# Kernel optimization log

Hardware: AMD Instinct MI355X
Metric: run time of the kernel (lower is better)

The kernel has to match this reference:

```python
import jax, jax.numpy as jnp
import numpy as np

ALPHA = 0.2  # leaky_relu negative slope


def setup_inputs() -> dict:
    key = jax.random.key(0)
    ks = jax.random.split(key, 6)
    N, E, F_IN, F_OUT, E_DIM = 50000, 800000, 256, 256, 64
    h = jax.random.normal(ks[0], (N, F_IN), dtype=jnp.float32)
    e_feat = jax.random.normal(ks[1], (E, E_DIM), dtype=jnp.float32)
    W = jax.random.normal(ks[2], (F_OUT, F_IN), dtype=jnp.float32) * (1.0 / np.sqrt(F_IN))
    A = jax.random.normal(ks[3], (1, 2 * F_OUT + E_DIM), dtype=jnp.float32) * 0.05
    src = jax.random.randint(ks[4], (E,), 0, N, dtype=jnp.int32)
    dst = jax.random.randint(ks[5], (E,), 0, N, dtype=jnp.int32)
    return {"h": h, "e_feat": e_feat, "W": W, "A": A, "src": src, "dst": dst}


def reference(h, e_feat, W, A, src, dst):
    N = h.shape[0]
    F_OUT = W.shape[0]
    # equation (1): node projection
    z = h @ W.T  # [N, F_OUT]
    z_src = z[src]  # [E, F_OUT]
    z_dst = z[dst]  # [E, F_OUT]
    # equation (2): per-edge attention logit = attn_fc([z_src, z_dst, e_feat])
    # split A to avoid materializing the [E, 2F+De] concat
    a_src, a_dst, a_e = A[0, :F_OUT], A[0, F_OUT:2 * F_OUT], A[0, 2 * F_OUT:]
    logits = z_src @ a_src + z_dst @ a_dst + e_feat @ a_e  # [E]
    e = jax.nn.leaky_relu(logits, ALPHA)
    # equations (3)&(4): segment-softmax over incoming edges per destination
    m = jax.ops.segment_max(e, dst, num_segments=N)  # [N]
    ex = jnp.exp(e - m[dst])
    denom = jax.ops.segment_sum(ex, dst, num_segments=N)  # [N]
    alpha = ex / denom[dst]  # [E]
    h_out = jax.ops.segment_sum(alpha[:, None] * z_src, dst, num_segments=N)
    return h_out
```

## Files before the change

kernel.cpp:

```cpp
#include <hip/hip_runtime.h>
#include <hip/hip_bf16.h>

#define FDIM 256
#define EDIM 64
#define LEAKY 0.2f

#define BM 128
#define BN 128
#define BK 32

typedef __attribute__((ext_vector_type(8))) short bfrag;
typedef __attribute__((ext_vector_type(4))) float f4acc;

__device__ __forceinline__ unsigned f2bf(float x){
    unsigned u = __float_as_uint(x);
    return (u + 0x7FFFu + ((u >> 16) & 1u)) >> 16;
}
__device__ __forceinline__ float bf2f(unsigned b){
    return __uint_as_float(b << 16);
}
__device__ __forceinline__ unsigned pack_hi(float x, float y, float& hx, float& hy){
    unsigned bx = f2bf(x), by = f2bf(y);
    hx = bf2f(bx); hy = bf2f(by);
    return bx | (by << 16);
}
__device__ __forceinline__ unsigned pack_lo(float rx, float ry){
    return f2bf(rx) | (f2bf(ry) << 16);
}

__device__ __forceinline__ void atomic_max_float(float* addr, float val){
    if (val >= 0.f) atomicMax((int*)addr, __float_as_int(val));
    else            atomicMin((unsigned int*)addr, (unsigned int)__float_as_int(val));
}

__global__ void k_init(float* __restrict__ m, float* __restrict__ s_src,
                       float* __restrict__ s_dst, int* __restrict__ counts, int N){
    int i = blockIdx.x*256 + threadIdx.x;
    if (i < N){
        m[i] = -3.402823466e38f;
        s_src[i] = 0.f; s_dst[i] = 0.f;
        counts[i] = 0;
    }
}

__global__ __launch_bounds__(256, 2) void k_gemm(const float* __restrict__ h,
                                                 const float* __restrict__ W,
                                                 const float* __restrict__ A,
                                                 unsigned short* __restrict__ z16,
                                                 float* __restrict__ s_src,
                                                 float* __restrict__ s_dst, int M){
    __shared__ uint4 smA[BM*8];
    __shared__ uint4 smB[BN*8];
    __shared__ float sred[2][2][BM];

    int tid = threadIdx.x;
    int m0 = blockIdx.x * BM;
    int n0 = blockIdx.y * BN;

    int wid  = tid >> 6;
    int lane = tid & 63;
    int wm = (wid >> 1) * 64;
    int wn = (wid & 1) * 64;
    int l15 = lane & 15;
    int l4  = lane >> 4;

    f4acc acc[4][4];
    #pragma unroll
    for (int i = 0; i < 4; ++i)
        #pragma unroll
        for (int j = 0; j < 4; ++j)
            acc[i][j] = (f4acc)(0.f);

    for (int kc = 0; kc < FDIM; kc += BK){
        #pragma unroll
        for (int q = 0; q < 4; ++q){
            int p = tid + q*256;
            int isB = p >= 512;
            int pp = p & 511;
            int row = pp >> 2, k8 = pp & 3;
            float4 v0, v1;
            if (isB){
                const float* g = &W[(n0 + row)*FDIM + kc + k8*8];
                v0 = *(const float4*)g; v1 = *(const float4*)(g + 4);
            } else {
                int gr = m0 + row;
                if (gr < M){
                    const float* g = &h[(size_t)gr*FDIM + kc + k8*8];
                    v0 = *(const float4*)g; v1 = *(const float4*)(g + 4);
                } else {
                    v0 = make_float4(0.f,0.f,0.f,0.f); v1 = v0;
                }
            }
            int sh = k8 ^ (row & 7);
            if (isB){
                uint4 hi; float hx, hy;
                hi.x = pack_hi(v0.x, v0.y, hx, hy);
                hi.y = pack_hi(v0.z, v0.w, hx, hy);
                hi.z = pack_hi(v1.x, v1.y, hx, hy);
                hi.w = pack_hi(v1.z, v1.w, hx, hy);
                smB[row*8 + sh] = hi;
            } else {
                uint4 hi, lo; float hx, hy;
                hi.x = pack_hi(v0.x, v0.y, hx, hy);
                lo.x = pack_lo(v0.x - hx, v0.y - hy);
                hi.y = pack_hi(v0.z, v0.w, hx, hy);
                lo.y = pack_lo(v0.z - hx, v0.w - hy);
                hi.z = pack_hi(v1.x, v1.y, hx, hy);
                lo.z = pack_lo(v1.x - hx, v1.y - hy);
                hi.w = pack_hi(v1.z, v1.w, hx, hy);
                lo.w = pack_lo(v1.z - hx, v1.w - hy);
                smA[row*8 + sh]       = hi;
                smA[row*8 + (sh ^ 4)] = lo;
            }
        }
        __syncthreads();

        bfrag ah[4], al[4];
        #pragma unroll
        for (int mf = 0; mf < 4; ++mf){
            int row = wm + mf*16 + l15;
            int sh = l4 ^ (row & 7);
            ah[mf] = *(const bfrag*)&smA[row*8 + sh];
            al[mf] = *(const bfrag*)&smA[row*8 + (sh ^ 4)];
        }
        #pragma unroll
        for (int nf = 0; nf < 4; ++nf){
            int row = wn + nf*16 + l15;
            int sh = l4 ^ (row & 7);
            bfrag bh = *(const bfrag*)&smB[row*8 + sh];
            #pragma unroll
            for (int mf = 0; mf < 4; ++mf){
                acc[mf][nf] = __builtin_amdgcn_mfma_f32_16x16x32_bf16(ah[mf], bh, acc[mf][nf], 0, 0, 0);
                acc[mf][nf] = __builtin_amdgcn_mfma_f32_16x16x32_bf16(al[mf], bh, acc[mf][nf], 0, 0, 0);
            }
        }
        __syncthreads();
    }

    #pragma unroll
    for (int mf = 0; mf < 4; ++mf){
        #pragma unroll
        for (int nf = 0; nf < 4; ++nf){
            int gcol = n0 + wn + nf*16 + l15;
            #pragma unroll
            for (int r = 0; r < 4; ++r){
                int grow = m0 + wm + mf*16 + l4*4 + r;
                if (grow < M)
                    z16[(size_t)grow*FDIM + gcol] = (unsigned short)f2bf(acc[mf][nf][r]);
            }
        }
    }

    float aS[4], aD[4];
    #pragma unroll
    for (int nf = 0; nf < 4; ++nf){
        int gcol = n0 + wn + nf*16 + l15;
        aS[nf] = A[gcol];
        aD[nf] = A[FDIM + gcol];
    }
    #pragma unroll
    for (int mf = 0; mf < 4; ++mf){
        #pragma unroll
        for (int r = 0; r < 4; ++r){
            float ps = 0.f, pd = 0.f;
            #pragma unroll
            for (int nf = 0; nf < 4; ++nf){
                ps += acc[mf][nf][r] * aS[nf];
                pd += acc[mf][nf][r] * aD[nf];
            }
            #pragma unroll
            for (int o = 1; o < 16; o <<= 1){
                ps += __shfl_xor(ps, o);
                pd += __shfl_xor(pd, o);
            }
            if (l15 == 0){
                int row = wm + mf*16 + l4*4 + r;
                sred[wid & 1][0][row] = ps;
                sred[wid & 1][1][row] = pd;
            }
        }
    }
    __syncthreads();
    if (tid < BM){
        int grow = m0 + tid;
        if (grow < M){
            atomicAdd(&s_src[grow], sred[0][0][tid] + sred[1][0][tid]);
            atomicAdd(&s_dst[grow], sred[0][1][tid] + sred[1][1][tid]);
        }
    }
}

__global__ void k_count(const int* __restrict__ dst, int* __restrict__ counts, int E){
    int e = blockIdx.x*256 + threadIdx.x;
    if (e < E) atomicAdd(&counts[dst[e]], 1);
}

__global__ void k_chunk_sums(const int* __restrict__ counts, int* __restrict__ bsums, int N){
    __shared__ int sh[256];
    int base = blockIdx.x*1024;
    int s = 0;
    for (int i = threadIdx.x; i < 1024; i += 256){
        int idx = base + i;
        s += (idx < N) ? counts[idx] : 0;
    }
    sh[threadIdx.x] = s; __syncthreads();
    for (int o = 128; o > 0; o >>= 1){
        if (threadIdx.x < o) sh[threadIdx.x] += sh[threadIdx.x + o];
        __syncthreads();
    }
    if (threadIdx.x == 0) bsums[blockIdx.x] = sh[0];
}

__global__ void k_scan_small(int* __restrict__ b, int nb){
    __shared__ int sh[1024];
    int tid = threadIdx.x;
    int v = (tid < nb) ? b[tid] : 0;
    sh[tid] = v; __syncthreads();
    int acc = v;
    for (int o = 1; o < 1024; o <<= 1){
        int t = (tid >= o) ? sh[tid - o] : 0;
        __syncthreads();
        acc += t; sh[tid] = acc;
        __syncthreads();
    }
    if (tid < nb) b[tid] = acc - v;
}

__global__ void k_scan_chunks(int* __restrict__ counts, int* __restrict__ cursor,
                              const int* __restrict__ bsums, int N, int E){
    __shared__ int sh[256];
    int tid = threadIdx.x;
    int base = blockIdx.x*1024 + tid*4;
    int v[4]; int s = 0;
    #pragma unroll
    for (int l = 0; l < 4; l++){
        int idx = base + l;
        v[l] = (idx < N) ? counts[idx] : 0;
        s += v[l];
    }
    sh[tid] = s; __syncthreads();
    int acc = s;
    for (int o = 1; o < 256; o <<= 1){
        int t = (tid >= o) ? sh[tid - o] : 0;
        __syncthreads();
        acc += t; sh[tid] = acc;
        __syncthreads();
    }
    int excl = acc - s + bsums[blockIdx.x];
    #pragma unroll
    for (int l = 0; l < 4; l++){
        int idx = base + l;
        if (idx < N){ counts[idx] = excl; cursor[idx] = excl; }
        excl += v[l];
    }
    if (blockIdx.x == 0 && tid == 0) counts[N] = E;
}

__global__ void k_edge(const float* __restrict__ ef, const float* __restrict__ A,
                       const float* __restrict__ s_src, const float* __restrict__ s_dst,
                       const int* __restrict__ src, const int* __restrict__ dst,
                       float* __restrict__ m, int* __restrict__ cursor,
                       int2* __restrict__ epair, int E){
    int gt = blockIdx.x*256 + threadIdx.x;
    int e = gt >> 4, l4 = gt & 15;
    if (e >= E) return;
    float4 f  = *(const float4*)&ef[(size_t)e*EDIM + l4*4];
    float4 ae = *(const float4*)&A[2*FDIM + l4*4];
    float v = f.x*ae.x + f.y*ae.y + f.z*ae.z + f.w*ae.w;
    v += __shfl_xor(v, 8); v += __shfl_xor(v, 4);
    v += __shfl_xor(v, 2); v += __shfl_xor(v, 1);
    if (l4 == 0){
        int d = dst[e];
        float lg = v + s_src[src[e]] + s_dst[d];
        lg = lg > 0.f ? lg : LEAKY*lg;
        atomic_max_float(&m[d], lg);
        int p = atomicAdd(&cursor[d], 1);
        int2 pr; pr.x = src[e]; pr.y = __float_as_int(lg);
        epair[p] = pr;
    }
}

__global__ __launch_bounds__(256) void k_out(const unsigned short* __restrict__ z16,
                                             const int* __restrict__ offsets,
                                             const int2* __restrict__ epair,
                                             const float* __restrict__ m,
                                             float* __restrict__ out, int N){
    int n = blockIdx.x*4 + (threadIdx.x >> 6);
    int lane = threadIdx.x & 63;
    if (n >= N) return;
    int i0 = offsets[n], i1 = offsets[n+1];
    float mx = m[n];

    float4 a[4];
    a[0] = make_float4(0,0,0,0); a[1] = a[0]; a[2] = a[0]; a[3] = a[0];
    float ds[4] = {0.f, 0.f, 0.f, 0.f};
    const unsigned short* zb = z16 + lane*4;

    int i = i0;
    for (; i + 7 < i1; i += 8){
        int2 p[8]; uint2 r[8];
        #pragma unroll
        for (int j = 0; j < 8; ++j) p[j] = epair[i+j];
        #pragma unroll
        for (int j = 0; j < 8; ++j) r[j] = *(const uint2*)&zb[(size_t)p[j].x*FDIM];
        #pragma unroll
        for (int j = 0; j < 8; ++j){
            float w = __expf(__int_as_float(p[j].y) - mx);
            ds[j & 3] += w;
            a[j & 3].x += w*bf2f(r[j].x & 0xffffu);
            a[j & 3].y += w*bf2f(r[j].x >> 16);
            a[j & 3].z += w*bf2f(r[j].y & 0xffffu);
            a[j & 3].w += w*bf2f(r[j].y >> 16);
        }
    }
    for (; i + 3 < i1; i += 4){
        int2 p[4]; uint2 r[4];
        #pragma unroll
        for (int j = 0; j < 4; ++j) p[j] = epair[i+j];
        #pragma unroll
        for (int j = 0; j < 4; ++j) r[j] = *(const uint2*)&zb[(size_t)p[j].x*FDIM];
        #pragma unroll
        for (int j = 0; j < 4; ++j){
            float w = __expf(__int_as_float(p[j].y) - mx);
            ds[j] += w;
            a[j].x += w*bf2f(r[j].x & 0xffffu);
            a[j].y += w*bf2f(r[j].x >> 16);
            a[j].z += w*bf2f(r[j].y & 0xffffu);
            a[j].w += w*bf2f(r[j].y >> 16);
        }
    }
    for (; i < i1; ++i){
        int2 p0 = epair[i];
        uint2 r0 = *(const uint2*)&zb[(size_t)p0.x*FDIM];
        float w = __expf(__int_as_float(p0.y) - mx);
        ds[0] += w;
        a[0].x += w*bf2f(r0.x & 0xffffu);
        a[0].y += w*bf2f(r0.x >> 16);
        a[0].z += w*bf2f(r0.y & 0xffffu);
        a[0].w += w*bf2f(r0.y >> 16);
    }
    float dsum = (ds[0] + ds[1]) + (ds[2] + ds[3]);
    float inv = (i1 > i0) ? 1.f / dsum : 0.f;
    float4 res;
    res.x = ((a[0].x + a[1].x) + (a[2].x + a[3].x)) * inv;
    res.y = ((a[0].y + a[1].y) + (a[2].y + a[3].y)) * inv;
    res.z = ((a[0].z + a[1].z) + (a[2].z + a[3].z)) * inv;
    res.w = ((a[0].w + a[1].w) + (a[2].w + a[3].w)) * inv;
    *(float4*)&out[(size_t)n*FDIM + lane*4] = res;
}

extern "C" void kernel_launch(void* const* d_in, const int* in_sizes, int n_in,
                              void* d_out, int out_size, void* d_ws, size_t ws_size,
                              hipStream_t stream){
    const float* h  = (const float*)d_in[0];
    const float* ef = (const float*)d_in[1];
    const float* W  = (const float*)d_in[2];
    const float* A  = (const float*)d_in[3];
    const int*  src = (const int*)d_in[4];
    const int*  dst = (const int*)d_in[5];
    float* out = (float*)d_out;
    int N = in_sizes[0] / FDIM;
    int E = in_sizes[4];

    char* ws = (char*)d_ws;
    size_t off = 0;
    auto alloc = [&](size_t nbytes)->char*{
        char* p = ws + off;
        off = (off + nbytes + 255) & ~(size_t)255;
        return p;
    };
    unsigned short* z16 = (unsigned short*)alloc((size_t)N*FDIM*2);
    float* s_src  = (float*)alloc((size_t)N*4);
    float* s_dst  = (float*)alloc((size_t)N*4);
    float* mbuf   = (float*)alloc((size_t)N*4);
    int*   counts = (int*)alloc((size_t)(N+1)*4);
    int*   cursor = (int*)alloc((size_t)N*4);
    int2*  epair  = (int2*)alloc((size_t)E*8);
    int*   bsums  = (int*)alloc(1024*4);

    int nb = (N + 1023)/1024;

    hipLaunchKernelGGL(k_init, dim3((N+255)/256), dim3(256), 0, stream,
                       mbuf, s_src, s_dst, counts, N);
    hipLaunchKernelGGL(k_gemm, dim3((N+BM-1)/BM, FDIM/BN), dim3(256), 0, stream,
                       h, W, A, z16, s_src, s_dst, N);
    hipLaunchKernelGGL(k_count, dim3((E+255)/256), dim3(256), 0, stream,
                       dst, counts, E);
    hipLaunchKernelGGL(k_chunk_sums, dim3(nb), dim3(256), 0, stream,
                       counts, bsums, N);
    hipLaunchKernelGGL(k_scan_small, dim3(1), dim3(1024), 0, stream,
                       bsums, nb);
    hipLaunchKernelGGL(k_scan_chunks, dim3(nb), dim3(256), 0, stream,
                       counts, cursor, bsums, N, E);
    hipLaunchKernelGGL(k_edge, dim3((E+15)/16), dim3(256), 0, stream,
                       ef, A, s_src, s_dst, src, dst, mbuf, cursor, epair, E);
    hipLaunchKernelGGL(k_out, dim3((N+3)/4), dim3(256), 0, stream,
                       z16, counts, epair, mbuf, out, N);
}
```

Before: 237.3 us.

## Compute per-node softmax max in output kernel instead of global atomics

```diff
diff --git a/kernel.cpp b/kernel.cpp
--- a/kernel.cpp
+++ b/kernel.cpp
@@ -28,19 +28,10 @@
     return f2bf(rx) | (f2bf(ry) << 16);
 }
 
-__device__ __forceinline__ void atomic_max_float(float* addr, float val){
-    if (val >= 0.f) atomicMax((int*)addr, __float_as_int(val));
-    else            atomicMin((unsigned int*)addr, (unsigned int)__float_as_int(val));
-}
-
-__global__ void k_init(float* __restrict__ m, float* __restrict__ s_src,
-                       float* __restrict__ s_dst, int* __restrict__ counts, int N){
+__global__ void k_init(float* __restrict__ s_src, float* __restrict__ s_dst,
+                       int* __restrict__ counts, int N){
     int i = blockIdx.x*256 + threadIdx.x;
-    if (i < N){
-        m[i] = -3.402823466e38f;
-        s_src[i] = 0.f; s_dst[i] = 0.f;
-        counts[i] = 0;
-    }
+    if (i < N){ s_src[i] = 0.f; s_dst[i] = 0.f; counts[i] = 0; }
 }
 
 __global__ __launch_bounds__(256, 2) void k_gemm(const float* __restrict__ h,
@@ -259,8 +250,7 @@
 __global__ void k_edge(const float* __restrict__ ef, const float* __restrict__ A,
                        const float* __restrict__ s_src, const float* __restrict__ s_dst,
                        const int* __restrict__ src, const int* __restrict__ dst,
-                       float* __restrict__ m, int* __restrict__ cursor,
-                       int2* __restrict__ epair, int E){
+                       int* __restrict__ cursor, int2* __restrict__ epair, int E){
     int gt = blockIdx.x*256 + threadIdx.x;
     int e = gt >> 4, l4 = gt & 15;
     if (e >= E) return;
@@ -273,7 +263,6 @@
         int d = dst[e];
         float lg = v + s_src[src[e]] + s_dst[d];
         lg = lg > 0.f ? lg : LEAKY*lg;
-        atomic_max_float(&m[d], lg);
         int p = atomicAdd(&cursor[d], 1);
         int2 pr; pr.x = src[e]; pr.y = __float_as_int(lg);
         epair[p] = pr;
@@ -283,64 +272,69 @@
 __global__ __launch_bounds__(256) void k_out(const unsigned short* __restrict__ z16,
                                              const int* __restrict__ offsets,
                                              const int2* __restrict__ epair,
-                                             const float* __restrict__ m,
                                              float* __restrict__ out, int N){
     int n = blockIdx.x*4 + (threadIdx.x >> 6);
     int lane = threadIdx.x & 63;
     if (n >= N) return;
     int i0 = offsets[n], i1 = offsets[n+1];
-    float mx = m[n];
+
+    float mlane = -3.402823466e38f;
+    for (int i = i0 + lane; i < i1; i += 64)
+        mlane = fmaxf(mlane, __int_as_float(epair[i].y));
+    float mx = mlane;
+    #pragma unroll
+    for (int o = 32; o > 0; o >>= 1)
+        mx = fmaxf(mx, __shfl_xor(mx, o));
 
     float4 a[4];
     a[0] = make_float4(0,0,0,0); a[1] = a[0]; a[2] = a[0]; a[3] = a[0];
-    float ds[4] = {0.f, 0.f, 0.f, 0.f};
+    float dw = 0.f;
     const unsigned short* zb = z16 + lane*4;
 
-    int i = i0;
-    for (; i + 7 < i1; i += 8){
-        int2 p[8]; uint2 r[8];
-        #pragma unroll
-        for (int j = 0; j < 8; ++j) p[j] = epair[i+j];
-        #pragma unroll
-        for (int j = 0; j < 8; ++j) r[j] = *(const uint2*)&zb[(size_t)p[j].x*FDIM];
-        #pragma unroll
-        for (int j = 0; j < 8; ++j){
-            float w = __expf(__int_as_float(p[j].y) - mx);
-            ds[j & 3] += w;
-            a[j & 3].x += w*bf2f(r[j].x & 0xffffu);
-            a[j & 3].y += w*bf2f(r[j].x >> 16);
-            a[j & 3].z += w*bf2f(r[j].y & 0xffffu);
-            a[j & 3].w += w*bf2f(r[j].y >> 16);
-        }
-    }
-    for (; i + 3 < i1; i += 4){
-        int2 p[4]; uint2 r[4];
-        #pragma unroll
-        for (int j = 0; j < 4; ++j) p[j] = epair[i+j];
-        #pragma unroll
-        for (int j = 0; j < 4; ++j) r[j] = *(const uint2*)&zb[(size_t)p[j].x*FDIM];
-        #pragma unroll
-        for (int j = 0; j < 4; ++j){
-            float w = __expf(__int_as_float(p[j].y) - mx);
-            ds[j] += w;
-            a[j].x += w*bf2f(r[j].x & 0xffffu);
-            a[j].y += w*bf2f(r[j].x >> 16);
-            a[j].z += w*bf2f(r[j].y & 0xffffu);
-            a[j].w += w*bf2f(r[j].y >> 16);
-        }
-    }
-    for (; i < i1; ++i){
-        int2 p0 = epair[i];
-        uint2 r0 = *(const uint2*)&zb[(size_t)p0.x*FDIM];
-        float w = __expf(__int_as_float(p0.y) - mx);
-        ds[0] += w;
-        a[0].x += w*bf2f(r0.x & 0xffffu);
-        a[0].y += w*bf2f(r0.x >> 16);
-        a[0].z += w*bf2f(r0.y & 0xffffu);
-        a[0].w += w*bf2f(r0.y >> 16);
-    }
-    float dsum = (ds[0] + ds[1]) + (ds[2] + ds[3]);
-    float inv = (i1 > i0) ? 1.f / dsum : 0.f;
+    for (int base = i0; base < i1; base += 64){
+        int cnt = min(64, i1 - base);
+        int2 pe = make_int2(0, 0);
+        float w = 0.f;
+        if (lane < cnt){
+            pe = epair[base + lane];
+            w = __expf(__int_as_float(pe.y) - mx);
+        }
+        dw += w;
+        int j = 0;
+        for (; j + 7 < cnt; j += 8){
+            float wj[8]; int sj[8]; uint2 rj[8];
+            #pragma unroll
+            for (int q = 0; q < 8; ++q){
+                wj[q] = __shfl(w, j + q);
+                sj[q] = __shfl(pe.x, j + q);
+            }
+            #pragma unroll
+            for (int q = 0; q < 8; ++q)
+                rj[q] = *(const uint2*)&zb[(size_t)sj[q]*FDIM];
+            #pragma unroll
+            for (int q = 0; q < 8; ++q){
+                a[q & 3].x += wj[q]*bf2f(rj[q].x & 0xffffu);
+                a[q & 3].y += wj[q]*bf2f(rj[q].x >> 16);
+                a[q & 3].z += wj[q]*bf2f(rj[q].y & 0xffffu);
+                a[q & 3].w += wj[q]*bf2f(rj[q].y >> 16);
+            }
+        }
+        for (; j < cnt; ++j){
+            float wq = __shfl(w, j);
+            int   sq = __shfl(pe.x, j);
+            uint2 r0 = *(const uint2*)&zb[(size_t)sq*FDIM];
+            a[0].x += wq*bf2f(r0.x & 0xffffu);
+            a[0].y += wq*bf2f(r0.x >> 16);
+            a[0].z += wq*bf2f(r0.y & 0xffffu);
+            a[0].w += wq*bf2f(r0.y >> 16);
+        }
+    }
+
+    #pragma unroll
+    for (int o = 32; o > 0; o >>= 1)
+        dw += __shfl_xor(dw, o);
+
+    float inv = (i1 > i0) ? 1.f / dw : 0.f;
     float4 res;
     res.x = ((a[0].x + a[1].x) + (a[2].x + a[3].x)) * inv;
     res.y = ((a[0].y + a[1].y) + (a[2].y + a[3].y)) * inv;
@@ -372,7 +366,6 @@
     unsigned short* z16 = (unsigned short*)alloc((size_t)N*FDIM*2);
     float* s_src  = (float*)alloc((size_t)N*4);
     float* s_dst  = (float*)alloc((size_t)N*4);
-    float* mbuf   = (float*)alloc((size_t)N*4);
     int*   counts = (int*)alloc((size_t)(N+1)*4);
     int*   cursor = (int*)alloc((size_t)N*4);
     int2*  epair  = (int2*)alloc((size_t)E*8);
@@ -381,7 +374,7 @@
     int nb = (N + 1023)/1024;
 
     hipLaunchKernelGGL(k_init, dim3((N+255)/256), dim3(256), 0, stream,
-                       mbuf, s_src, s_dst, counts, N);
+                       s_src, s_dst, counts, N);
     hipLaunchKernelGGL(k_gemm, dim3((N+BM-1)/BM, FDIM/BN), dim3(256), 0, stream,
                        h, W, A, z16, s_src, s_dst, N);
     hipLaunchKernelGGL(k_count, dim3((E+255)/256), dim3(256), 0, stream,
@@ -393,7 +386,7 @@
     hipLaunchKernelGGL(k_scan_chunks, dim3(nb), dim3(256), 0, stream,
                        counts, cursor, bsums, N, E);
     hipLaunchKernelGGL(k_edge, dim3((E+15)/16), dim3(256), 0, stream,
-                       ef, A, s_src, s_dst, src, dst, mbuf, cursor, epair, E);
+                       ef, A, s_src, s_dst, src, dst, cursor, epair, E);
     hipLaunchKernelGGL(k_out, dim3((N+3)/4), dim3(256), 0, stream,
-                       z16, counts, epair, mbuf, out, N);
-}
+                       z16, counts, epair, out, N);
+}
```

Result: faster. 230.4 us (-2.9%).
